# Kernel optimization log

Hardware: AMD Instinct MI355X
Metric: run time of the kernel (lower is better)

Reference implementation:

```python
import jax, jax.numpy as jnp
import numpy as np

EMBED_DIM = 1024
NUM_HEADS = 16
HEAD_DIM = EMBED_DIM // NUM_HEADS
LN_EPS = 1e-5


def setup_inputs() -> dict:
    key = jax.random.key(0)
    ks = jax.random.split(key, 13)
    b, n_q, k_len, E = 4, 2048, 2048, EMBED_DIM
    s = 1.0 / np.sqrt(E)
    inp = {
        "Q_input": jax.random.normal(ks[0], (b, n_q, E), jnp.float32),
        "K_input": jax.random.normal(ks[1], (b, k_len, E), jnp.float32),
        "V_input": jax.random.normal(ks[2], (b, k_len, E), jnp.float32),
        "Wq": jax.random.normal(ks[3], (E, E), jnp.float32) * s,
        "bq": jnp.zeros((E,), jnp.float32),
        "Wk": jax.random.normal(ks[4], (E, E), jnp.float32) * s,
        "bk": jnp.zeros((E,), jnp.float32),
        "Wv": jax.random.normal(ks[5], (E, E), jnp.float32) * s,
        "bv": jnp.zeros((E,), jnp.float32),
        "Wo": jax.random.normal(ks[6], (E, E), jnp.float32) * s,
        "bo": jnp.zeros((E,), jnp.float32),
        "gamma": jnp.ones((E,), jnp.float32),
        "beta": jnp.zeros((E,), jnp.float32),
    }
    return inp


def _layer_norm(x, gamma, beta):
    mu = jnp.mean(x, axis=-1, keepdims=True)
    var = jnp.mean(jnp.square(x - mu), axis=-1, keepdims=True)
    return (x - mu) * jax.lax.rsqrt(var + LN_EPS) * gamma + beta


def reference(Q_input, K_input, V_input, Wq, bq, Wk, bk, Wv, bv, Wo, bo, gamma, beta):
    b, n_q, E = Q_input.shape
    k_len = K_input.shape[1]
    H, D = NUM_HEADS, HEAD_DIM
    # projections (Linear: x @ W^T + b; here W stored as [E_in, E_out])
    Q = (Q_input @ Wq + bq).reshape(b, n_q, H, D).transpose(0, 2, 1, 3)   # [b,H,n_q,D]
    K = (K_input @ Wk + bk).reshape(b, k_len, H, D).transpose(0, 2, 1, 3)  # [b,H,k,D]
    V = (V_input @ Wv + bv).reshape(b, k_len, H, D).transpose(0, 2, 1, 3)
    scores = jnp.einsum('bhqd,bhkd->bhqk', Q, K) / jnp.sqrt(jnp.float32(D))
    attn = jax.nn.softmax(scores, axis=-1)
    ctx = jnp.einsum('bhqk,bhkd->bhqd', attn, V)           # [b,H,n_q,D]
    ctx = ctx.transpose(0, 2, 1, 3).reshape(b, n_q, E)
    out = ctx @ Wo + bo                                    # dropout = identity (eval)
    return _layer_norm(Q_input + out, gamma, beta)
```

## Files before the change

### kernel.cpp

```cpp
#include <hip/hip_runtime.h>

typedef __attribute__((ext_vector_type(8))) short s8v;
typedef __attribute__((ext_vector_type(4))) short s4v;
typedef __attribute__((ext_vector_type(4))) float f4v;

#define MFMA16(a, b, c) __builtin_amdgcn_mfma_f32_16x16x32_bf16((a), (b), (c), 0, 0, 0)
#define AS1 __attribute__((address_space(1)))
#define AS3 __attribute__((address_space(3)))

__device__ __forceinline__ short f2bf(float f) {
  union { float f; unsigned u; } v; v.f = f;
  unsigned r = v.u + 0x7FFFu + ((v.u >> 16) & 1u);
  return (short)(r >> 16);
}
__device__ __forceinline__ float bf2f(short s) {
  union { unsigned u; float f; } v; v.u = ((unsigned)(unsigned short)s) << 16;
  return v.f;
}
__device__ __forceinline__ unsigned fbits(float f) {
  union { float f; unsigned u; } v; v.f = f; return v.u;
}
__device__ __forceinline__ unsigned pack2(float hi, float lo) {
  return __builtin_amdgcn_perm(fbits(hi), fbits(lo), 0x07060302u);
}
__device__ __forceinline__ void gld16(const void* g, void* l) {
  __builtin_amdgcn_global_load_lds((const AS1 unsigned*)g, (AS3 unsigned*)l, 16, 0, 0);
}

__global__ __launch_bounds__(256) void wtrans4(const float* __restrict__ W0,
                                               const float* __restrict__ W1,
                                               const float* __restrict__ W2,
                                               const float* __restrict__ W3,
                                               short* __restrict__ Wt) {
  const float* W = blockIdx.z == 0 ? W0 : blockIdx.z == 1 ? W1 : blockIdx.z == 2 ? W2 : W3;
  Wt += (size_t)blockIdx.z * 1048576;
  __shared__ float tile[64][65];
  const int r0 = blockIdx.y * 64, c0 = blockIdx.x * 64;
  const int t = threadIdx.x;
  for (int i = 0; i < 4; ++i) {
    int lin = t + i * 256;
    int row = lin >> 4, c4 = (lin & 15) << 2;
    float4 v = *(const float4*)(W + (size_t)(r0 + row) * 1024 + c0 + c4);
    tile[row][c4 + 0] = v.x; tile[row][c4 + 1] = v.y;
    tile[row][c4 + 2] = v.z; tile[row][c4 + 3] = v.w;
  }
  __syncthreads();
  for (int i = 0; i < 4; ++i) {
    int lin = t + i * 256;
    int nl = lin >> 4, k4 = (lin & 15) << 2;
    s4v sv = { f2bf(tile[k4 + 0][nl]), f2bf(tile[k4 + 1][nl]),
               f2bf(tile[k4 + 2][nl]), f2bf(tile[k4 + 3][nl]) };
    *(s4v*)&Wt[(size_t)(c0 + nl) * 1024 + r0 + k4] = sv;
  }
}

template <int CAST, int EPI>
__global__ __launch_bounds__(256) void gemm_bt(
    const float* __restrict__ Af0, const float* __restrict__ Af1,
    const float* __restrict__ Af2, const short* __restrict__ Ab,
    const short* __restrict__ Bt,
    const float* __restrict__ b0, const float* __restrict__ b1,
    const float* __restrict__ b2, float s0,
    short* __restrict__ outb) {
  __shared__ __align__(16) short smem[17408];

  const int z = blockIdx.z;
  const float* Af = (CAST && z == 1) ? Af1 : (CAST && z == 2) ? Af2 : Af0;
  Bt += (size_t)z * 1048576;
  outb += (size_t)z * 8388608;
  const float* bias = z == 0 ? b0 : z == 1 ? b1 : b2;
  const float scale = z == 0 ? s0 : 1.f;

  const int tid = threadIdx.x;
  const int lane = tid & 63, w = tid >> 6;
  const int quad = lane >> 4, l16 = lane & 15;
  const int wm = (w >> 1) * 64, wn = (w & 1) * 64;
  const int mBase = blockIdx.x * 128, nBase = blockIdx.y * 128;
  f4v acc[4][4] = {};

  const int id0 = tid, id1 = tid + 256;
  const short* Bg0 = Bt + (size_t)((id0 >> 2) + nBase) * 1024 + ((id0 & 3) << 3);
  const short* Bg1 = Bt + (size_t)((id1 >> 2) + nBase) * 1024 + ((id1 & 3) << 3);
  const short* Ag0 = nullptr; const short* Ag1 = nullptr;
  const float* Ap[4];
  int Aslot[4];
  if constexpr (CAST) {
#pragma unroll
    for (int i = 0; i < 4; ++i) {
      int id = tid + i * 256;
      Ap[i] = Af + (size_t)(mBase + (id >> 3)) * 1024 + ((id & 7) << 2);
      Aslot[i] = (id >> 3) * 32 + ((id & 7) << 2);
    }
  } else {
    Ag0 = Ab + (size_t)((id0 >> 2) + mBase) * 1024 + ((id0 & 3) << 3);
    Ag1 = Ab + (size_t)((id1 >> 2) + mBase) * 1024 + ((id1 & 3) << 3);
  }

  float4 apre[4];
  if constexpr (CAST) {
#pragma unroll
    for (int i = 0; i < 4; ++i) apre[i] = *(const float4*)(Ap[i]);
#pragma unroll
    for (int i = 0; i < 4; ++i) {
      s4v sv = { f2bf(apre[i].x), f2bf(apre[i].y), f2bf(apre[i].z), f2bf(apre[i].w) };
      *(s4v*)&smem[Aslot[i]] = sv;
    }
#pragma unroll
    for (int i = 0; i < 4; ++i) apre[i] = *(const float4*)(Ap[i] + 32);
  } else {
    gld16(Ag0, &smem[id0 * 8]);
    gld16(Ag1, &smem[id1 * 8]);
  }
  gld16(Bg0, &smem[4096 + id0 * 8]);
  gld16(Bg1, &smem[4096 + id1 * 8]);

  for (int kt = 0; kt < 32; ++kt) {
    const int bo_ = (kt & 1) * 8192, nbo = bo_ ^ 8192;
    __syncthreads();
    if (kt < 31) {
      gld16(Bg0 + (kt + 1) * 32, &smem[nbo + 4096 + id0 * 8]);
      gld16(Bg1 + (kt + 1) * 32, &smem[nbo + 4096 + id1 * 8]);
      if constexpr (CAST) {
#pragma unroll
        for (int i = 0; i < 4; ++i) {
          s4v sv = { f2bf(apre[i].x), f2bf(apre[i].y), f2bf(apre[i].z), f2bf(apre[i].w) };
          *(s4v*)&smem[nbo + Aslot[i]] = sv;
        }
        if (kt < 30) {
#pragma unroll
          for (int i = 0; i < 4; ++i) apre[i] = *(const float4*)(Ap[i] + (kt + 2) * 32);
        }
      } else {
        gld16(Ag0 + (kt + 1) * 32, &smem[nbo + id0 * 8]);
        gld16(Ag1 + (kt + 1) * 32, &smem[nbo + id1 * 8]);
      }
    }
    s8v a[4], b[4];
#pragma unroll
    for (int mt = 0; mt < 4; ++mt) a[mt] = *(const s8v*)&smem[bo_ + (wm + mt * 16 + l16) * 32 + quad * 8];
#pragma unroll
    for (int nt = 0; nt < 4; ++nt) b[nt] = *(const s8v*)&smem[bo_ + 4096 + (wn + nt * 16 + l16) * 32 + quad * 8];
#pragma unroll
    for (int mt = 0; mt < 4; ++mt)
#pragma unroll
      for (int nt = 0; nt < 4; ++nt)
        acc[mt][nt] = MFMA16(a[mt], b[nt], acc[mt][nt]);
  }

  __syncthreads();
  const int bI = mBase >> 11, tok0 = mBase & 2047;
  const bool vpath = (EPI == 0) && (z == 2);
  short (*Ta)[136] = (short(*)[136])smem;
  short (*Tv)[136] = (short(*)[136])smem;
  if (vpath) {
#pragma unroll
    for (int nt = 0; nt < 4; ++nt) {
      int featl = wn + nt * 16 + l16;
      float bs = bias[nBase + featl];
#pragma unroll
      for (int mt = 0; mt < 4; ++mt) {
        union { s4v v; unsigned u[2]; } pk;
        pk.u[0] = pack2(acc[mt][nt][1] + bs, acc[mt][nt][0] + bs);
        pk.u[1] = pack2(acc[mt][nt][3] + bs, acc[mt][nt][2] + bs);
        *(s4v*)&Tv[featl][wm + mt * 16 + quad * 4] = pk.v;
      }
    }
  } else {
#pragma unroll
    for (int nt = 0; nt < 4; ++nt) {
      int featl = wn + nt * 16 + l16;
      float bs = bias[nBase + featl];
#pragma unroll
      for (int mt = 0; mt < 4; ++mt)
#pragma unroll
        for (int r = 0; r < 4; ++r)
          Ta[wm + mt * 16 + quad * 4 + r][featl] = f2bf((acc[mt][nt][r] + bs) * scale);
    }
  }
  __syncthreads();
  if (vpath) {
#pragma unroll
    for (int it = 0; it < 8; ++it) {
      int id = tid + it * 256;
      int f = id >> 4, t8 = (id & 15) << 3;
      s8v v = *(const s8v*)&Tv[f][t8];
      int gf = nBase + f, h = gf >> 6, d = gf & 63;
      *(s8v*)&outb[(((size_t)bI * 16 + h) * 64 + d) * 2048 + tok0 + t8] = v;
    }
  } else {
#pragma unroll
    for (int it = 0; it < 8; ++it) {
      int id = tid + it * 256;
      int tok = id >> 4, f8 = (id & 15) << 3;
      s8v v = *(const s8v*)&Ta[tok][f8];
      if constexpr (EPI == 1) {
        *(s8v*)&outb[(size_t)(mBase + tok) * 1024 + nBase + f8] = v;
      } else {
        int gf = nBase + f8, h = gf >> 6, d = gf & 63;
        *(s8v*)&outb[(((size_t)bI * 16 + h) * 2048 + tok0 + tok) * 64 + d] = v;
      }
    }
  }
}

__global__ __launch_bounds__(256, 2) void attn_kernel(
    const short* __restrict__ Qp, const short* __restrict__ Kp,
    const short* __restrict__ Vpt, short* __restrict__ Ctx) {
  __shared__ __align__(16) short Ks[64][72];
  __shared__ __align__(16) short Vt[64][72];

  const int tid = threadIdx.x, w = tid >> 6, lane = tid & 63;
  const int quad = lane >> 4, l16 = lane & 15;
  const int qt = blockIdx.x, bh = blockIdx.y;
  const short* Qb = Qp + (size_t)bh * 2048 * 64;
  const short* Kb = Kp + (size_t)bh * 2048 * 64;
  const short* Vb = Vpt + (size_t)bh * 64 * 2048;
  const int qbase = qt * 256 + w * 64;

  s8v qf[4][2];
#pragma unroll
  for (int mt = 0; mt < 4; ++mt)
#pragma unroll
    for (int h = 0; h < 2; ++h)
      qf[mt][h] = *(const s8v*)(Qb + (size_t)(qbase + mt * 16 + l16) * 64 + h * 32 + quad * 8);

  const s8v vone = {16256, 16256, 16256, 16256, 16256, 16256, 16256, 16256};
  f4v Oa[4][4] = {};
  f4v La[4] = {};

  for (int kv = 0; kv < 32; ++kv) {
    const int kv0 = kv * 64;
    __syncthreads();
#pragma unroll
    for (int i = 0; i < 2; ++i) {
      int id = tid + i * 256;
      int g = id >> 3, c8 = (id & 7) << 3;
      int p = (g & 32) | (((g >> 2) & 1) << 4) | (((g >> 3) & 3) << 2) | (g & 3);
      *(s8v*)&Ks[p][c8] = *(const s8v*)(Kb + (size_t)(kv0 + g) * 64 + c8);
      *(s8v*)&Vt[g][c8] = *(const s8v*)(Vb + (size_t)g * 2048 + kv0 + c8);
    }
    __syncthreads();

    s8v kf[4][2], vf[4][2];
#pragma unroll
    for (int T = 0; T < 4; ++T) {
      kf[T][0] = *(const s8v*)&Ks[T * 16 + l16][quad * 8];
      kf[T][1] = *(const s8v*)&Ks[T * 16 + l16][32 + quad * 8];
      vf[T][0] = *(const s8v*)&Vt[T * 16 + l16][quad * 8];
      vf[T][1] = *(const s8v*)&Vt[T * 16 + l16][32 + quad * 8];
    }

#pragma unroll
    for (int mt = 0; mt < 4; ++mt) {
      f4v s[4] = {};
#pragma unroll
      for (int T = 0; T < 4; ++T) {
        s[T] = MFMA16(kf[T][0], qf[mt][0], s[T]);
        s[T] = MFMA16(kf[T][1], qf[mt][1], s[T]);
      }
#pragma unroll
      for (int T = 0; T < 4; ++T)
#pragma unroll
        for (int r = 0; r < 4; ++r)
          s[T][r] = __builtin_amdgcn_exp2f(s[T][r]);
      s8v pf[2];
#pragma unroll
      for (int cp = 0; cp < 2; ++cp) {
        union { s8v v; unsigned u[4]; } pk;
        pk.u[0] = pack2(s[2 * cp][1], s[2 * cp][0]);
        pk.u[1] = pack2(s[2 * cp][3], s[2 * cp][2]);
        pk.u[2] = pack2(s[2 * cp + 1][1], s[2 * cp + 1][0]);
        pk.u[3] = pack2(s[2 * cp + 1][3], s[2 * cp + 1][2]);
        pf[cp] = pk.v;
      }
      La[mt] = MFMA16(pf[0], vone, La[mt]);
      La[mt] = MFMA16(pf[1], vone, La[mt]);
#pragma unroll
      for (int nt = 0; nt < 4; ++nt) {
        Oa[mt][nt] = MFMA16(pf[0], vf[nt][0], Oa[mt][nt]);
        Oa[mt][nt] = MFMA16(pf[1], vf[nt][1], Oa[mt][nt]);
      }
    }
  }

  const int b = bh >> 4, h = bh & 15;
#pragma unroll
  for (int mt = 0; mt < 4; ++mt)
#pragma unroll
    for (int r = 0; r < 4; ++r) {
      float inv = 1.f / La[mt][r];
      int q = qbase + mt * 16 + quad * 4 + r;
#pragma unroll
      for (int nt = 0; nt < 4; ++nt) {
        int d = nt * 16 + l16;
        Ctx[((size_t)b * 2048 + q) * 1024 + h * 64 + d] = f2bf(Oa[mt][nt][r] * inv);
      }
    }
}

__global__ __launch_bounds__(256) void ln_kernel(
    const float* __restrict__ resid, const short* __restrict__ attnb,
    const float* __restrict__ gamma, const float* __restrict__ beta,
    float* __restrict__ out) {
  const int row = blockIdx.x, t = threadIdx.x;
  const float4 rv = *(const float4*)(resid + (size_t)row * 1024 + t * 4);
  const s4v av = *(const s4v*)(attnb + (size_t)row * 1024 + t * 4);
  float x0 = rv.x + bf2f(av[0]), x1 = rv.y + bf2f(av[1]);
  float x2 = rv.z + bf2f(av[2]), x3 = rv.w + bf2f(av[3]);
  float s = x0 + x1 + x2 + x3;
  float ss = x0 * x0 + x1 * x1 + x2 * x2 + x3 * x3;
  for (int off = 32; off > 0; off >>= 1) {
    s += __shfl_down(s, off, 64);
    ss += __shfl_down(ss, off, 64);
  }
  __shared__ float red[8];
  const int wid = t >> 6, lane = t & 63;
  if (lane == 0) { red[wid] = s; red[4 + wid] = ss; }
  __syncthreads();
  float S = red[0] + red[1] + red[2] + red[3];
  float SS = red[4] + red[5] + red[6] + red[7];
  float mu = S * (1.f / 1024.f);
  float var = SS * (1.f / 1024.f) - mu * mu;
  float rstd = rsqrtf(var + 1e-5f);
  const float4 g = *(const float4*)(gamma + t * 4);
  const float4 bb = *(const float4*)(beta + t * 4);
  float4 o;
  o.x = (x0 - mu) * rstd * g.x + bb.x;
  o.y = (x1 - mu) * rstd * g.y + bb.y;
  o.z = (x2 - mu) * rstd * g.z + bb.z;
  o.w = (x3 - mu) * rstd * g.w + bb.w;
  *(float4*)(out + (size_t)row * 1024 + t * 4) = o;
}

extern "C" void kernel_launch(void* const* d_in, const int* in_sizes, int n_in,
                              void* d_out, int out_size, void* d_ws, size_t ws_size,
                              hipStream_t stream) {
  const float* Qin = (const float*)d_in[0];
  const float* Kin = (const float*)d_in[1];
  const float* Vin = (const float*)d_in[2];
  const float* Wq = (const float*)d_in[3];
  const float* bq = (const float*)d_in[4];
  const float* Wk = (const float*)d_in[5];
  const float* bk = (const float*)d_in[6];
  const float* Wv = (const float*)d_in[7];
  const float* bv = (const float*)d_in[8];
  const float* Wo = (const float*)d_in[9];
  const float* bo = (const float*)d_in[10];
  const float* gamma = (const float*)d_in[11];
  const float* beta = (const float*)d_in[12];
  float* out = (float*)d_out;

  char* ws = (char*)d_ws;
  const size_t MB = 1024 * 1024;
  short* Qp    = (short*)(ws);
  short* Ctx   = (short*)(ws + 48 * MB);
  short* AOutB = (short*)(ws + 64 * MB);
  short* Wt    = (short*)(ws + 80 * MB);

  wtrans4<<<dim3(16, 16, 4), 256, 0, stream>>>(Wq, Wk, Wv, Wo, Wt);

  const float qscale = 0.125f * 1.44269504f;

  gemm_bt<1, 0><<<dim3(64, 8, 3), 256, 0, stream>>>(
      Qin, Kin, Vin, nullptr, Wt, bq, bk, bv, qscale, Qp);

  attn_kernel<<<dim3(8, 64), 256, 0, stream>>>(Qp, Qp + 8388608, Qp + 16777216, Ctx);

  gemm_bt<0, 1><<<dim3(64, 8, 1), 256, 0, stream>>>(
      nullptr, nullptr, nullptr, Ctx, Wt + 3 * 1048576, bo, bo, bo, 1.f, AOutB);

  ln_kernel<<<8192, 256, 0, stream>>>(Qin, AOutB, gamma, beta, out);
}
```

Baseline: 348.8 us.

## Double-buffer K/V tiles in attention and simplify bf16 cast packing in GEMM

The attention kernel now keeps two shared-memory buffers for K and V. It prefetches the next tile into registers before the barrier and writes it to the alternate buffer after the MFMA work, so only one barrier per iteration remains and global load latency overlaps compute. Separately, the fp32-to-bf16 conversion in the casting GEMM path now uses a cheaper round-half-up add plus a perm-pack instead of full round-to-nearest-even per element. This changes rounding slightly at ties, and the double-buffering raises register and LDS pressure, which could affect occupancy at two blocks per CU.

```diff
diff --git a/kernel.cpp b/kernel.cpp
--- a/kernel.cpp
+++ b/kernel.cpp
@@ -22,6 +22,9 @@
 }
 __device__ __forceinline__ unsigned pack2(float hi, float lo) {
   return __builtin_amdgcn_perm(fbits(hi), fbits(lo), 0x07060302u);
+}
+__device__ __forceinline__ unsigned pack2rn(float hi, float lo) {
+  return __builtin_amdgcn_perm(fbits(hi) + 0x8000u, fbits(lo) + 0x8000u, 0x07060302u);
 }
 __device__ __forceinline__ void gld16(const void* g, void* l) {
   __builtin_amdgcn_global_load_lds((const AS1 unsigned*)g, (AS3 unsigned*)l, 16, 0, 0);
@@ -102,8 +105,10 @@
     for (int i = 0; i < 4; ++i) apre[i] = *(const float4*)(Ap[i]);
 #pragma unroll
     for (int i = 0; i < 4; ++i) {
-      s4v sv = { f2bf(apre[i].x), f2bf(apre[i].y), f2bf(apre[i].z), f2bf(apre[i].w) };
-      *(s4v*)&smem[Aslot[i]] = sv;
+      union { s4v v; unsigned u[2]; } pk;
+      pk.u[0] = pack2rn(apre[i].y, apre[i].x);
+      pk.u[1] = pack2rn(apre[i].w, apre[i].z);
+      *(s4v*)&smem[Aslot[i]] = pk.v;
     }
 #pragma unroll
     for (int i = 0; i < 4; ++i) apre[i] = *(const float4*)(Ap[i] + 32);
@@ -123,8 +128,10 @@
       if constexpr (CAST) {
 #pragma unroll
         for (int i = 0; i < 4; ++i) {
-          s4v sv = { f2bf(apre[i].x), f2bf(apre[i].y), f2bf(apre[i].z), f2bf(apre[i].w) };
-          *(s4v*)&smem[nbo + Aslot[i]] = sv;
+          union { s4v v; unsigned u[2]; } pk;
+          pk.u[0] = pack2rn(apre[i].y, apre[i].x);
+          pk.u[1] = pack2rn(apre[i].w, apre[i].z);
+          *(s4v*)&smem[nbo + Aslot[i]] = pk.v;
         }
         if (kt < 30) {
 #pragma unroll
@@ -206,8 +213,8 @@
 __global__ __launch_bounds__(256, 2) void attn_kernel(
     const short* __restrict__ Qp, const short* __restrict__ Kp,
     const short* __restrict__ Vpt, short* __restrict__ Ctx) {
-  __shared__ __align__(16) short Ks[64][72];
-  __shared__ __align__(16) short Vt[64][72];
+  __shared__ __align__(16) short Ks[2][64][72];
+  __shared__ __align__(16) short Vt[2][64][72];
 
   const int tid = threadIdx.x, w = tid >> 6, lane = tid & 63;
   const int quad = lane >> 4, l16 = lane & 15;
@@ -217,37 +224,60 @@
   const short* Vb = Vpt + (size_t)bh * 64 * 2048;
   const int qbase = qt * 256 + w * 64;
 
+  int sg[2], sc8[2], sp[2];
+  const short* Ksrc[2];
+  const short* Vsrc[2];
+#pragma unroll
+  for (int i = 0; i < 2; ++i) {
+    int id = tid + i * 256;
+    int g = id >> 3, c8 = (id & 7) << 3;
+    int p = (g & 32) | (((g >> 2) & 1) << 4) | (((g >> 3) & 3) << 2) | (g & 3);
+    sg[i] = g; sc8[i] = c8; sp[i] = p;
+    Ksrc[i] = Kb + (size_t)g * 64 + c8;
+    Vsrc[i] = Vb + (size_t)g * 2048 + c8;
+  }
+
   s8v qf[4][2];
 #pragma unroll
   for (int mt = 0; mt < 4; ++mt)
 #pragma unroll
     for (int h = 0; h < 2; ++h)
       qf[mt][h] = *(const s8v*)(Qb + (size_t)(qbase + mt * 16 + l16) * 64 + h * 32 + quad * 8);
+
+  {
+    s8v kr[2], vr[2];
+#pragma unroll
+    for (int i = 0; i < 2; ++i) { kr[i] = *(const s8v*)Ksrc[i]; vr[i] = *(const s8v*)Vsrc[i]; }
+#pragma unroll
+    for (int i = 0; i < 2; ++i) {
+      *(s8v*)&Ks[0][sp[i]][sc8[i]] = kr[i];
+      *(s8v*)&Vt[0][sg[i]][sc8[i]] = vr[i];
+    }
+  }
 
   const s8v vone = {16256, 16256, 16256, 16256, 16256, 16256, 16256, 16256};
   f4v Oa[4][4] = {};
   f4v La[4] = {};
 
   for (int kv = 0; kv < 32; ++kv) {
-    const int kv0 = kv * 64;
+    const int buf = kv & 1;
+    s8v kn[2], vn[2];
+    if (kv < 31) {
+#pragma unroll
+      for (int i = 0; i < 2; ++i) {
+        kn[i] = *(const s8v*)(Ksrc[i] + (size_t)(kv + 1) * 4096);
+        vn[i] = *(const s8v*)(Vsrc[i] + (size_t)(kv + 1) * 64);
+      }
+    }
     __syncthreads();
-#pragma unroll
-    for (int i = 0; i < 2; ++i) {
-      int id = tid + i * 256;
-      int g = id >> 3, c8 = (id & 7) << 3;
-      int p = (g & 32) | (((g >> 2) & 1) << 4) | (((g >> 3) & 3) << 2) | (g & 3);
-      *(s8v*)&Ks[p][c8] = *(const s8v*)(Kb + (size_t)(kv0 + g) * 64 + c8);
-      *(s8v*)&Vt[g][c8] = *(const s8v*)(Vb + (size_t)g * 2048 + kv0 + c8);
-    }
-    __syncthreads();
 
     s8v kf[4][2], vf[4][2];
 #pragma unroll
     for (int T = 0; T < 4; ++T) {
-      kf[T][0] = *(const s8v*)&Ks[T * 16 + l16][quad * 8];
-      kf[T][1] = *(const s8v*)&Ks[T * 16 + l16][32 + quad * 8];
-      vf[T][0] = *(const s8v*)&Vt[T * 16 + l16][quad * 8];
-      vf[T][1] = *(const s8v*)&Vt[T * 16 + l16][32 + quad * 8];
+      kf[T][0] = *(const s8v*)&Ks[buf][T * 16 + l16][quad * 8];
+      kf[T][1] = *(const s8v*)&Ks[buf][T * 16 + l16][32 + quad * 8];
+      vf[T][0] = *(const s8v*)&Vt[buf][T * 16 + l16][quad * 8];
+      vf[T][1] = *(const s8v*)&Vt[buf][T * 16 + l16][32 + quad * 8];
     }
 
 #pragma unroll
@@ -279,6 +309,14 @@
       for (int nt = 0; nt < 4; ++nt) {
         Oa[mt][nt] = MFMA16(pf[0], vf[nt][0], Oa[mt][nt]);
         Oa[mt][nt] = MFMA16(pf[1], vf[nt][1], Oa[mt][nt]);
+      }
+    }
+
+    if (kv < 31) {
+#pragma unroll
+      for (int i = 0; i < 2; ++i) {
+        *(s8v*)&Ks[buf ^ 1][sp[i]][sc8[i]] = kn[i];
+        *(s8v*)&Vt[buf ^ 1][sg[i]][sc8[i]] = vn[i];
       }
     }
   }
```

Result: no change. 348.6 us (-0.1%).
